# Optimization experiments

Measured on AMD Instinct MI355X. Metric: run time of the kernel, lower is better.

## Reference

```python
import jax, jax.numpy as jnp
import numpy as np
import math

B, T, IN_DIM = 4, 1024, 64
D, H, L, DFF = 1024, 16, 4, 4096
N_STEPS = 24
MAXLEN = 2048
DK = D // H


def _pos_encoding(max_len, d):
    pos = np.arange(max_len, dtype=np.float32)[:, None]
    div = np.exp(np.arange(0, d, 2, dtype=np.float32) * (-math.log(10000.0) / d))
    pe = np.zeros((max_len, d), dtype=np.float32)
    pe[:, 0::2] = np.sin(pos * div)
    pe[:, 1::2] = np.cos(pos * div)
    return jnp.asarray(pe)

_PE = _pos_encoding(MAXLEN, D)


def _lin(x, W, b):
    # torch Linear convention: W is (out, in)
    return x @ W.T + b


def _mha(q, kv, Wq, bq, Wk, bk, Wv, bv, Wo, bo):
    Bq, Tq, _ = q.shape
    Tk = kv.shape[1]
    Qh = _lin(q, Wq, bq).reshape(Bq, Tq, H, DK).transpose(0, 2, 1, 3)
    Kh = _lin(kv, Wk, bk).reshape(Bq, Tk, H, DK).transpose(0, 2, 1, 3)
    Vh = _lin(kv, Wv, bv).reshape(Bq, Tk, H, DK).transpose(0, 2, 1, 3)
    scores = jnp.einsum('bhqd,bhkd->bhqk', Qh, Kh) / math.sqrt(DK)
    probs = jax.nn.softmax(scores, axis=-1)
    out = jnp.einsum('bhqk,bhkd->bhqd', probs, Vh)
    out = out.transpose(0, 2, 1, 3).reshape(Bq, Tq, D)
    return _lin(out, Wo, bo)


def _ffn(x, W1, b1, W2, b2):
    return _lin(jax.nn.relu(_lin(x, W1, b1)), W2, b2)


def _ln(x, g, b, eps=1e-5):
    mu = jnp.mean(x, axis=-1, keepdims=True)
    var = jnp.var(x, axis=-1, keepdims=True)
    return (x - mu) / jnp.sqrt(var + eps) * g + b


def setup_inputs() -> dict:
    key = jax.random.key(0)
    ks = iter(jax.random.split(key, 64))
    def w(shape, s=0.02):
        return jax.random.normal(next(ks), shape, jnp.float32) * s
    inp = {'x': jax.random.normal(next(ks), (B, T, IN_DIM), jnp.float32)}
    inp['in_W'] = w((D, IN_DIM)); inp['in_b'] = jnp.zeros((D,), jnp.float32)
    for p in ['enc', 'dec']:
        for n in ['Wq', 'Wk', 'Wv', 'Wo']:
            inp[f'{p}_{n}'] = w((L, D, D))
            inp[f'{p}_b{n[1].lower()}'] = jnp.zeros((L, D), jnp.float32)
    for p in ['ffe', 'ffd']:
        inp[f'{p}_W1'] = w((DFF, D)); inp[f'{p}_b1'] = jnp.zeros((DFF,), jnp.float32)
        inp[f'{p}_W2'] = w((D, DFF)); inp[f'{p}_b2'] = jnp.zeros((D,), jnp.float32)
    for p in ['ne', 'nd']:
        inp[f'{p}_g'] = jnp.ones((D,), jnp.float32); inp[f'{p}_b'] = jnp.zeros((D,), jnp.float32)
    inp['out_W'] = w((1, D)); inp['out_b'] = jnp.zeros((1,), jnp.float32)
    inp['temb_W'] = w((D, 1)); inp['temb_b'] = jnp.zeros((D,), jnp.float32)
    return inp


def reference(x, in_W, in_b,
              enc_Wq, enc_bq, enc_Wk, enc_bk, enc_Wv, enc_bv, enc_Wo, enc_bo,
              ffe_W1, ffe_b1, ffe_W2, ffe_b2, ne_g, ne_b,
              dec_Wq, dec_bq, dec_Wk, dec_bk, dec_Wv, dec_bv, dec_Wo, dec_bo,
              ffd_W1, ffd_b1, ffd_W2, ffd_b2, nd_g, nd_b,
              out_W, out_b, temb_W, temb_b):
    batch, seq, _ = x.shape
    h = _lin(x, in_W, in_b) + _PE[:seq]
    for l in range(L):
        h = _mha(h, h, enc_Wq[l], enc_bq[l], enc_Wk[l], enc_bk[l],
                 enc_Wv[l], enc_bv[l], enc_Wo[l], enc_bo[l])
        h = _ln(h + _ffn(h, ffe_W1, ffe_b1, ffe_W2, ffe_b2), ne_g, ne_b)
    dec = jnp.zeros((batch, 1, D), x.dtype)
    preds = []
    for _ in range(N_STEPS):
        d = dec + _PE[:dec.shape[1]]
        for l in range(L):
            # same layer weights used for self- and cross-attention, as in source
            d = _mha(d, d, dec_Wq[l], dec_bq[l], dec_Wk[l], dec_bk[l],
                     dec_Wv[l], dec_bv[l], dec_Wo[l], dec_bo[l])
            d = _mha(d, h, dec_Wq[l], dec_bq[l], dec_Wk[l], dec_bk[l],
                     dec_Wv[l], dec_bv[l], dec_Wo[l], dec_bo[l])
            d = _ln(d + _ffn(d, ffd_W1, ffd_b1, ffd_W2, ffd_b2), nd_g, nd_b)
        step = _lin(d[:, -1, :], out_W, out_b)        # (B, 1)
        preds.append(step[:, None, :])                 # (B, 1, 1)
        emb = _lin(step, temb_W, temb_b)[:, None, :]   # (B, 1, D)
        dec = jnp.concatenate([dec, emb], axis=1)
    return jnp.concatenate(preds, axis=1)              # (B, n_steps, 1)
```

## Files before the change

### kernel.cpp

```cpp
#include <hip/hip_runtime.h>
#include <math.h>

#define DM    1024
#define NH    16
#define DKH   64
#define NL    4
#define DFFN  4096
#define BB    4
#define TT    1024
#define NSTEP 24
#define BT    (BB*TT)
#define MD    (BB*NSTEP)
#define CSPLIT 8
#define CKEYS  (TT/CSPLIT)

typedef __attribute__((ext_vector_type(8))) short s16x8;
typedef __attribute__((ext_vector_type(4))) short s16x4;
typedef __attribute__((ext_vector_type(4))) float f32x4;

__device__ inline short f2b(float f){
  unsigned u = __float_as_uint(f);
  u += 0x7fffu + ((u>>16)&1u);
  return (short)(u>>16);
}
__device__ inline float b2f(short h){
  return __uint_as_float(((unsigned)(unsigned short)h)<<16);
}

__global__ __launch_bounds__(256)
void split_kernel(const float* __restrict__ X, short* __restrict__ Hi,
                  short* __restrict__ Lo, int n8)
{
  const size_t i = (size_t)blockIdx.x*256 + threadIdx.x;
  if (i >= (size_t)n8) return;
  const float4 v0 = *(const float4*)(X + i*8);
  const float4 v1 = *(const float4*)(X + i*8 + 4);
  const float f[8] = {v0.x,v0.y,v0.z,v0.w,v1.x,v1.y,v1.z,v1.w};
  s16x8 hv, lv;
  #pragma unroll
  for (int e=0;e<8;e++){
    const short h = f2b(f[e]);
    hv[e] = h;
    lv[e] = f2b(f[e] - b2f(h));
  }
  *(s16x8*)(Hi + i*8) = hv;
  *(s16x8*)(Lo + i*8) = lv;
}

__global__ void zero_kernel(float* __restrict__ p, int n) {
  int i = blockIdx.x*256 + threadIdx.x;
  if (i < n) p[i] = 0.f;
}

__global__ __launch_bounds__(256)
void add_pe_split(const float* __restrict__ h, short* __restrict__ Hi,
                  short* __restrict__ Lo)
{
  const int row = blockIdx.x;
  const int pos = row & (TT-1);
  const int d = threadIdx.x*4;
  const float4 a = *(const float4*)(h + (size_t)row*DM + d);
  const float c1 = -9.210340371976184f / 1024.0f;
  const float e0 = expf((float)d * c1);
  const float e1 = expf((float)(d+2) * c1);
  const float a0 = (float)pos * e0, a1 = (float)pos * e1;
  const float v[4] = {a.x + sinf(a0), a.y + cosf(a0), a.z + sinf(a1), a.w + cosf(a1)};
  s16x4 hv, lv;
  #pragma unroll
  for (int e=0;e<4;e++){
    const short hb = f2b(v[e]);
    hv[e] = hb;
    lv[e] = f2b(v[e] - b2f(hb));
  }
  *(s16x4*)(Hi + (size_t)row*DM + d) = hv;
  *(s16x4*)(Lo + (size_t)row*DM + d) = lv;
}

__global__ __launch_bounds__(256)
void dec_prep_split(short* __restrict__ Dhi, short* __restrict__ Dlo,
                    const float* __restrict__ tok)
{
  const int r = blockIdx.x;
  const int i = r >> 2;
  const int d = threadIdx.x*4;
  const float4 a = *(const float4*)(tok + (size_t)r*DM + d);
  const float c1 = -9.210340371976184f / 1024.0f;
  const float e0 = expf((float)d * c1);
  const float e1 = expf((float)(d+2) * c1);
  const float a0 = (float)i * e0, a1 = (float)i * e1;
  const float v[4] = {a.x + sinf(a0), a.y + cosf(a0), a.z + sinf(a1), a.w + cosf(a1)};
  s16x4 hv, lv;
  #pragma unroll
  for (int e=0;e<4;e++){
    const short hb = f2b(v[e]);
    hv[e] = hb;
    lv[e] = f2b(v[e] - b2f(hb));
  }
  *(s16x4*)(Dhi + (size_t)r*DM + d) = hv;
  *(s16x4*)(Dlo + (size_t)r*DM + d) = lv;
}

template<int ACT, int OUT_MODE>
__global__ __launch_bounds__(256, 2)
void gemm_split(const short* __restrict__ Ahi, const short* __restrict__ Alo,
                const short* __restrict__ Bhi, const short* __restrict__ Blo,
                const float* __restrict__ bias,
                float* __restrict__ C, short* __restrict__ Chi, short* __restrict__ Clo,
                int M, int N, int K)
{
  __shared__ __align__(16) short lA[2][128][40];
  __shared__ __align__(16) short lB[2][128][40];
  const int tid = threadIdx.x;
  const int m0 = blockIdx.x*128, n0 = blockIdx.y*128;
  const int lane = tid & 63, w = tid >> 6;
  const int wr = w >> 1, wc = w & 1;
  const int fr = lane & 15, fq = lane >> 4;

  f32x4 acc[4][4];
  #pragma unroll
  for (int i=0;i<4;i++)
    #pragma unroll
    for (int j=0;j<4;j++) acc[i][j] = (f32x4){0.f,0.f,0.f,0.f};

  for (int k0 = 0; k0 < K; k0 += 32) {
    __syncthreads();
    #pragma unroll
    for (int j=0;j<2;j++){
      const int cc = tid + j*256;
      const int row = cc >> 2, kq = cc & 3;
      const size_t ga = (size_t)(m0+row)*K + k0 + kq*8;
      const size_t gb = (size_t)(n0+row)*K + k0 + kq*8;
      *(s16x8*)&lA[0][row][kq*8] = *(const s16x8*)(Ahi + ga);
      *(s16x8*)&lA[1][row][kq*8] = *(const s16x8*)(Alo + ga);
      *(s16x8*)&lB[0][row][kq*8] = *(const s16x8*)(Bhi + gb);
      *(s16x8*)&lB[1][row][kq*8] = *(const s16x8*)(Blo + gb);
    }
    __syncthreads();
    s16x8 ah[4], al[4], bh[4], bl[4];
    #pragma unroll
    for (int i=0;i<4;i++){
      ah[i] = *(const s16x8*)&lA[0][wr*64+i*16+fr][fq*8];
      al[i] = *(const s16x8*)&lA[1][wr*64+i*16+fr][fq*8];
    }
    #pragma unroll
    for (int j=0;j<4;j++){
      bh[j] = *(const s16x8*)&lB[0][wc*64+j*16+fr][fq*8];
      bl[j] = *(const s16x8*)&lB[1][wc*64+j*16+fr][fq*8];
    }
    #pragma unroll
    for (int i=0;i<4;i++)
      #pragma unroll
      for (int j=0;j<4;j++){
        acc[i][j] = __builtin_amdgcn_mfma_f32_16x16x32_bf16(ah[i], bh[j], acc[i][j], 0,0,0);
        acc[i][j] = __builtin_amdgcn_mfma_f32_16x16x32_bf16(ah[i], bl[j], acc[i][j], 0,0,0);
        acc[i][j] = __builtin_amdgcn_mfma_f32_16x16x32_bf16(al[i], bh[j], acc[i][j], 0,0,0);
      }
  }
  #pragma unroll
  for (int j=0;j<4;j++){
    const int col = n0 + wc*64 + j*16 + fr;
    const float bv = bias[col];
    #pragma unroll
    for (int i=0;i<4;i++){
      const int row0 = m0 + wr*64 + i*16 + fq*4;
      #pragma unroll
      for (int r=0;r<4;r++){
        float v = acc[i][j][r] + bv;
        if (ACT==1) v = fmaxf(v, 0.f);
        const size_t idx = (size_t)(row0+r)*N + col;
        if (OUT_MODE==0 || OUT_MODE==2) C[idx] = v;
        if (OUT_MODE==1 || OUT_MODE==2){
          const short hb = f2b(v);
          Chi[idx] = hb;
          Clo[idx] = f2b(v - b2f(hb));
        }
        if (OUT_MODE==3) Chi[idx] = f2b(v);
      }
    }
  }
}

template<int MR>
__global__ __launch_bounds__(256)
void gemm_dec(const short* __restrict__ Ahi, const short* __restrict__ Alo,
              const short* __restrict__ B0hi, const short* __restrict__ B0lo,
              const short* __restrict__ B1hi, const short* __restrict__ B1lo,
              const short* __restrict__ B2hi, const short* __restrict__ B2lo,
              float* __restrict__ part, int N, int K, int KS)
{
  const short* Bhi = (blockIdx.z==0) ? B0hi : (blockIdx.z==1 ? B1hi : B2hi);
  const short* Blo = (blockIdx.z==0) ? B0lo : (blockIdx.z==1 ? B1lo : B2lo);
  float* P = part + ((size_t)blockIdx.z*KS + blockIdx.y)*(size_t)MD*N;
  const int KK = K / KS;
  const int kbase = blockIdx.y * KK;
  const int n0 = blockIdx.x * 128;
  __shared__ __align__(16) short lA[2][96][40];
  __shared__ __align__(16) short lB[2][128][40];
  const int tid = threadIdx.x;
  const int lane = tid & 63, w = tid >> 6;
  const int fr = lane & 15, fq = lane >> 4;
  constexpr int CH = MR*128;

  f32x4 acc[MR][2];
  #pragma unroll
  for (int i=0;i<MR;i++){ acc[i][0]=(f32x4){0,0,0,0}; acc[i][1]=(f32x4){0,0,0,0}; }

  for (int k0 = kbase; k0 < kbase + KK; k0 += 32) {
    __syncthreads();
    #pragma unroll
    for (int t=0; t<(CH+255)/256; t++){
      const int cc = tid + t*256;
      if (cc < CH){
        const int row = cc>>3, hl = (cc>>2)&1, kq = cc&3;
        const short* src = hl ? Alo : Ahi;
        *(s16x8*)&lA[hl][row][kq*8] = *(const s16x8*)(src + (size_t)row*K + k0 + kq*8);
      }
    }
    #pragma unroll
    for (int t=0; t<4; t++){
      const int cc = tid + t*256;
      const int row = cc>>3, hl = (cc>>2)&1, kq = cc&3;
      const short* src = hl ? Blo : Bhi;
      *(s16x8*)&lB[hl][row][kq*8] = *(const s16x8*)(src + (size_t)(n0+row)*K + k0 + kq*8);
    }
    __syncthreads();
    s16x8 bh[2], bl[2];
    #pragma unroll
    for (int j=0;j<2;j++){
      bh[j] = *(const s16x8*)&lB[0][w*32+j*16+fr][fq*8];
      bl[j] = *(const s16x8*)&lB[1][w*32+j*16+fr][fq*8];
    }
    #pragma unroll
    for (int i=0;i<MR;i++){
      const s16x8 ah = *(const s16x8*)&lA[0][i*16+fr][fq*8];
      const s16x8 al = *(const s16x8*)&lA[1][i*16+fr][fq*8];
      #pragma unroll
      for (int j=0;j<2;j++){
        acc[i][j] = __builtin_amdgcn_mfma_f32_16x16x32_bf16(ah, bh[j], acc[i][j], 0,0,0);
        acc[i][j] = __builtin_amdgcn_mfma_f32_16x16x32_bf16(ah, bl[j], acc[i][j], 0,0,0);
        acc[i][j] = __builtin_amdgcn_mfma_f32_16x16x32_bf16(al, bh[j], acc[i][j], 0,0,0);
      }
    }
  }
  #pragma unroll
  for (int j=0;j<2;j++){
    const int col = n0 + w*32 + j*16 + fr;
    #pragma unroll
    for (int i=0;i<MR;i++){
      const int row0 = i*16 + fq*4;
      #pragma unroll
      for (int r=0;r<4;r++)
        P[(size_t)(row0+r)*N + col] = acc[i][j][r];
    }
  }
}

template<int ACT, int MODE>
__global__ __launch_bounds__(256)
void reduce_dec(const float* __restrict__ part,
                const float* __restrict__ b0, const float* __restrict__ b1,
                const float* __restrict__ b2,
                float* __restrict__ o0, float* __restrict__ o1, float* __restrict__ o2,
                short* __restrict__ ohi, short* __restrict__ olo,
                int N, int KS)
{
  const int idx = blockIdx.x*256 + threadIdx.x;
  const int z = blockIdx.y;
  const float* P = part + (size_t)z*KS*(size_t)MD*N;
  const float* bias = (z==0)?b0:(z==1?b1:b2);
  float* out = (z==0)?o0:(z==1?o1:o2);
  float s = 0.f;
  for (int ks=0; ks<KS; ks++) s += P[(size_t)ks*MD*N + idx];
  s += bias[idx & (N-1)];
  if (ACT==1) s = fmaxf(s, 0.f);
  if (MODE==0 || MODE==2) out[idx] = s;
  if (MODE==1 || MODE==2){
    if (z==0){
      const short hb = f2b(s);
      ohi[idx] = hb;
      olo[idx] = f2b(s - b2f(hb));
    }
  }
}

__global__ __launch_bounds__(256)
void attn_enc(const float* __restrict__ Qg, const float* __restrict__ Kg,
              const float* __restrict__ Vg, short* __restrict__ Ohi,
              short* __restrict__ Olo)
{
  const int bh = blockIdx.y;
  const int b = bh >> 4, hh = bh & 15;
  const int row = blockIdx.x*256 + threadIdx.x;
  const size_t base = ((size_t)b*TT)*DM + hh*DKH;
  float q[64];
  {
    const float* qp = Qg + base + (size_t)row*DM;
    #pragma unroll
    for (int d4=0; d4<16; d4++){
      const float4 v = *(const float4*)(qp + d4*4);
      q[d4*4+0]=v.x; q[d4*4+1]=v.y; q[d4*4+2]=v.z; q[d4*4+3]=v.w;
    }
  }
  float o[64];
  #pragma unroll
  for (int d=0;d<64;d++) o[d]=0.f;
  float m = -INFINITY, l = 0.f;
  __shared__ float Ks[64][68];
  __shared__ float Vs[64][68];
  for (int kt=0; kt<TT; kt+=64) {
    __syncthreads();
    #pragma unroll
    for (int t=0;t<4;t++){
      const int fi = threadIdx.x + t*256;
      const int j = fi>>4, dq = fi&15;
      *(float4*)&Ks[j][dq*4] = *(const float4*)(Kg + base + (size_t)(kt+j)*DM + dq*4);
      *(float4*)&Vs[j][dq*4] = *(const float4*)(Vg + base + (size_t)(kt+j)*DM + dq*4);
    }
    __syncthreads();
    for (int j=0;j<64;j++){
      float s0=0.f,s1=0.f,s2=0.f,s3=0.f;
      #pragma unroll
      for (int d=0; d<64; d+=4){
        s0 = fmaf(q[d+0], Ks[j][d+0], s0);
        s1 = fmaf(q[d+1], Ks[j][d+1], s1);
        s2 = fmaf(q[d+2], Ks[j][d+2], s2);
        s3 = fmaf(q[d+3], Ks[j][d+3], s3);
      }
      const float s = ((s0+s1)+(s2+s3)) * 0.125f;
      if (s > m) {
        const float f = __expf(m - s);
        l *= f;
        #pragma unroll
        for (int d=0;d<64;d++) o[d] *= f;
        m = s;
      }
      const float p = __expf(s - m);
      l += p;
      #pragma unroll
      for (int d=0;d<64;d++) o[d] = fmaf(p, Vs[j][d], o[d]);
    }
  }
  const float inv = 1.f / l;
  #pragma unroll
  for (int d8=0; d8<8; d8++){
    s16x8 hv, lv;
    #pragma unroll
    for (int e=0;e<8;e++){
      const float f = o[d8*8+e]*inv;
      const short hb = f2b(f);
      hv[e] = hb;
      lv[e] = f2b(f - b2f(hb));
    }
    *(s16x8*)(Ohi + base + (size_t)row*DM + d8*8) = hv;
    *(s16x8*)(Olo + base + (size_t)row*DM + d8*8) = lv;
  }
}

__global__ __launch_bounds__(256)
void attn_dec_selfp(const float* __restrict__ Qg, const float* __restrict__ Kg,
                    const float* __restrict__ Vg, short* __restrict__ Ohi,
                    short* __restrict__ Olo, int n)
{
  const int b = blockIdx.x >> 4, hh = blockIdx.x & 15;
  const size_t base = (size_t)b*DM + hh*DKH;
  __shared__ float Qs[NSTEP][68], Ks[NSTEP][68], Vs[NSTEP][68];
  __shared__ float P[NSTEP][28];
  const int tid = threadIdx.x;
  for (int t = tid; t < 3*n*16; t += 256) {
    const int tensor = t / (n*16);
    const int fi = t - tensor*(n*16);
    const int row = fi >> 4, dq = fi & 15;
    const float* src = (tensor==0?Qg:(tensor==1?Kg:Vg)) + base + (size_t)(row*4)*DM + dq*4;
    float (*dst)[68] = (tensor==0?Qs:(tensor==1?Ks:Vs));
    *(float4*)&dst[row][dq*4] = *(const float4*)src;
  }
  __syncthreads();
  for (int idx = tid; idx < n*n; idx += 256) {
    const int i = idx / n, j = idx - i*n;
    float s0=0.f,s1=0.f,s2=0.f,s3=0.f;
    #pragma unroll
    for (int d=0; d<64; d+=4){
      s0 = fmaf(Qs[i][d+0], Ks[j][d+0], s0);
      s1 = fmaf(Qs[i][d+1], Ks[j][d+1], s1);
      s2 = fmaf(Qs[i][d+2], Ks[j][d+2], s2);
      s3 = fmaf(Qs[i][d+3], Ks[j][d+3], s3);
    }
    P[i][j] = ((s0+s1)+(s2+s3))*0.125f;
  }
  __syncthreads();
  if (tid < n) {
    float mm = -INFINITY;
    for (int j=0;j<n;j++) mm = fmaxf(mm, P[tid][j]);
    float l = 0.f;
    for (int j=0;j<n;j++){ const float p = __expf(P[tid][j]-mm); P[tid][j]=p; l+=p; }
    const float inv = 1.f/l;
    for (int j=0;j<n;j++) P[tid][j] *= inv;
  }
  __syncthreads();
  for (int idx = tid; idx < n*64; idx += 256){
    const int i = idx >> 6, d = idx & 63;
    float s = 0.f;
    for (int j=0;j<n;j++) s = fmaf(P[i][j], Vs[j][d], s);
    const short hb = f2b(s);
    const size_t o = base + (size_t)(i*4)*DM + d;
    Ohi[o] = hb;
    Olo[o] = f2b(s - b2f(hb));
  }
}

__global__ __launch_bounds__(256)
void attn_cross_part(const float* __restrict__ Qg, const short* __restrict__ Kc,
                     const short* __restrict__ Vc, float* __restrict__ opart,
                     float* __restrict__ mlpart, int n)
{
  const int ks = blockIdx.x;
  const int bh = blockIdx.y;
  const int b = bh >> 4, hh = bh & 15;
  __shared__ float Qs[NSTEP][68];
  __shared__ float KVs[CKEYS][68];
  __shared__ float S[NSTEP][CKEYS+4];
  const int tid = threadIdx.x;
  const size_t qbase = (size_t)b*DM + hh*DKH;
  for (int t=tid; t<n*16; t+=256){
    const int row = t>>4, dq = t&15;
    *(float4*)&Qs[row][dq*4] = *(const float4*)(Qg + qbase + (size_t)(row*4)*DM + dq*4);
  }
  const size_t kbase = ((size_t)b*TT + (size_t)ks*CKEYS)*DM + hh*DKH;
  for (int t=tid; t<CKEYS*8; t+=256){
    const int row = t>>3, d8 = t&7;
    const s16x8 v = *(const s16x8*)(Kc + kbase + (size_t)row*DM + d8*8);
    #pragma unroll
    for (int e=0;e<8;e++) KVs[row][d8*8+e] = b2f(v[e]);
  }
  __syncthreads();
  for (int idx=tid; idx<n*128; idx+=256){
    const int i = idx >> 7, j = idx & 127;
    float s0=0.f,s1=0.f,s2=0.f,s3=0.f;
    #pragma unroll
    for (int d=0; d<64; d+=4){
      s0 = fmaf(Qs[i][d+0], KVs[j][d+0], s0);
      s1 = fmaf(Qs[i][d+1], KVs[j][d+1], s1);
      s2 = fmaf(Qs[i][d+2], KVs[j][d+2], s2);
      s3 = fmaf(Qs[i][d+3], KVs[j][d+3], s3);
    }
    S[i][j] = ((s0+s1)+(s2+s3))*0.125f;
  }
  __syncthreads();
  for (int t=tid; t<CKEYS*8; t+=256){
    const int row = t>>3, d8 = t&7;
    const s16x8 v = *(const s16x8*)(Vc + kbase + (size_t)row*DM + d8*8);
    #pragma unroll
    for (int e=0;e<8;e++) KVs[row][d8*8+e] = b2f(v[e]);
  }
  if (tid < n){
    float mm=-INFINITY;
    for (int j=0;j<CKEYS;j++) mm = fmaxf(mm, S[tid][j]);
    float l=0.f;
    for (int j=0;j<CKEYS;j++){ const float p=__expf(S[tid][j]-mm); S[tid][j]=p; l+=p; }
    mlpart[((size_t)bh*CSPLIT+ks)*(2*NSTEP) + tid*2+0] = mm;
    mlpart[((size_t)bh*CSPLIT+ks)*(2*NSTEP) + tid*2+1] = l;
  }
  __syncthreads();
  for (int idx=tid; idx<n*64; idx+=256){
    const int i = idx >> 6, d = idx & 63;
    float s=0.f;
    for (int j=0;j<CKEYS;j++) s = fmaf(S[i][j], KVs[j][d], s);
    opart[(((size_t)bh*CSPLIT+ks)*NSTEP + i)*DKH + d] = s;
  }
}

__global__ __launch_bounds__(256)
void attn_cross_comb(const float* __restrict__ opart, const float* __restrict__ mlpart,
                     short* __restrict__ Ohi, short* __restrict__ Olo, int n)
{
  const int bh = blockIdx.x;
  const int idx = blockIdx.y*256 + threadIdx.x;
  const int i = idx >> 6, d = idx & 63;
  if (i >= n) return;
  float M = -INFINITY;
  #pragma unroll
  for (int s=0;s<CSPLIT;s++)
    M = fmaxf(M, mlpart[((size_t)bh*CSPLIT+s)*(2*NSTEP) + i*2]);
  float acc = 0.f, L = 0.f;
  #pragma unroll
  for (int s=0;s<CSPLIT;s++){
    const float mm = mlpart[((size_t)bh*CSPLIT+s)*(2*NSTEP) + i*2+0];
    const float ll = mlpart[((size_t)bh*CSPLIT+s)*(2*NSTEP) + i*2+1];
    const float f = __expf(mm - M);
    acc = fmaf(f, opart[(((size_t)bh*CSPLIT+s)*NSTEP + i)*DKH + d], acc);
    L   = fmaf(f, ll, L);
  }
  const int b = bh >> 4, hh = bh & 15;
  const float v = acc / L;
  const short hb = f2b(v);
  const size_t o = ((size_t)(i*4+b))*DM + hh*DKH + d;
  Ohi[o] = hb;
  Olo[o] = f2b(v - b2f(hb));
}

__device__ inline float wave_sum(float v){
  #pragma unroll
  for (int off=1; off<64; off<<=1) v += __shfl_xor(v, off, 64);
  return v;
}

__global__ __launch_bounds__(256)
void ln_add_split(const float* __restrict__ X, const float* __restrict__ Y,
                  const float* __restrict__ g, const float* __restrict__ be,
                  short* __restrict__ Ohi, short* __restrict__ Olo)
{
  const size_t row = blockIdx.x;
  const int tid = threadIdx.x;
  const float4 a = *(const float4*)(X + row*DM + tid*4);
  const float4 b = *(const float4*)(Y + row*DM + tid*4);
  const float v0=a.x+b.x, v1=a.y+b.y, v2=a.z+b.z, v3=a.w+b.w;
  float s = v0+v1+v2+v3;
  float q = v0*v0+v1*v1+v2*v2+v3*v3;
  s = wave_sum(s); q = wave_sum(q);
  __shared__ float rs[4], rq[4];
  if ((tid&63)==0){ rs[tid>>6]=s; rq[tid>>6]=q; }
  __syncthreads();
  const float S = rs[0]+rs[1]+rs[2]+rs[3];
  const float Q = rq[0]+rq[1]+rq[2]+rq[3];
  const float mean = S * (1.f/DM);
  const float var  = Q * (1.f/DM) - mean*mean;
  const float rstd = rsqrtf(var + 1e-5f);
  const float4 gv = *(const float4*)(g  + tid*4);
  const float4 bv = *(const float4*)(be + tid*4);
  const float v[4] = {(v0-mean)*rstd*gv.x + bv.x, (v1-mean)*rstd*gv.y + bv.y,
                      (v2-mean)*rstd*gv.z + bv.z, (v3-mean)*rstd*gv.w + bv.w};
  s16x4 hv, lv;
  #pragma unroll
  for (int e=0;e<4;e++){
    const short hb = f2b(v[e]);
    hv[e] = hb;
    lv[e] = f2b(v[e] - b2f(hb));
  }
  *(s16x4*)(Ohi + row*DM + tid*4) = hv;
  *(s16x4*)(Olo + row*DM + tid*4) = lv;
}

__global__ __launch_bounds__(256)
void ln_add_dec(const float* __restrict__ X, const float* __restrict__ Y,
                const float* __restrict__ g, const float* __restrict__ be,
                float* __restrict__ Outf, short* __restrict__ Ohi,
                short* __restrict__ Olo)
{
  const size_t row = blockIdx.x;
  const int tid = threadIdx.x;
  const float4 a = *(const float4*)(X + row*DM + tid*4);
  const float4 b = *(const float4*)(Y + row*DM + tid*4);
  const float v0=a.x+b.x, v1=a.y+b.y, v2=a.z+b.z, v3=a.w+b.w;
  float s = v0+v1+v2+v3;
  float q = v0*v0+v1*v1+v2*v2+v3*v3;
  s = wave_sum(s); q = wave_sum(q);
  __shared__ float rs[4], rq[4];
  if ((tid&63)==0){ rs[tid>>6]=s; rq[tid>>6]=q; }
  __syncthreads();
  const float S = rs[0]+rs[1]+rs[2]+rs[3];
  const float Q = rq[0]+rq[1]+rq[2]+rq[3];
  const float mean = S * (1.f/DM);
  const float var  = Q * (1.f/DM) - mean*mean;
  const float rstd = rsqrtf(var + 1e-5f);
  const float4 gv = *(const float4*)(g  + tid*4);
  const float4 bv = *(const float4*)(be + tid*4);
  const float v[4] = {(v0-mean)*rstd*gv.x + bv.x, (v1-mean)*rstd*gv.y + bv.y,
                      (v2-mean)*rstd*gv.z + bv.z, (v3-mean)*rstd*gv.w + bv.w};
  float4 of; of.x=v[0]; of.y=v[1]; of.z=v[2]; of.w=v[3];
  *(float4*)(Outf + row*DM + tid*4) = of;
  s16x4 hv, lv;
  #pragma unroll
  for (int e=0;e<4;e++){
    const short hb = f2b(v[e]);
    hv[e] = hb;
    lv[e] = f2b(v[e] - b2f(hb));
  }
  *(s16x4*)(Ohi + row*DM + tid*4) = hv;
  *(s16x4*)(Olo + row*DM + tid*4) = lv;
}

__global__ __launch_bounds__(256)
void out_step(const float* __restrict__ Dv, const float* __restrict__ outW,
              const float* __restrict__ outB, const float* __restrict__ tembW,
              const float* __restrict__ tembB, float* __restrict__ dout,
              float* __restrict__ tok, int s)
{
  const int b = blockIdx.x;
  const int tid = threadIdx.x;
  const float* drow = Dv + ((size_t)(s*4 + b))*DM;
  const float4 dv = *(const float4*)(drow + tid*4);
  const float4 wv = *(const float4*)(outW + tid*4);
  float part = dv.x*wv.x + dv.y*wv.y + dv.z*wv.z + dv.w*wv.w;
  part = wave_sum(part);
  __shared__ float red[4];
  __shared__ float stepv;
  if ((tid&63)==0) red[tid>>6] = part;
  __syncthreads();
  if (tid==0) stepv = red[0]+red[1]+red[2]+red[3] + outB[0];
  __syncthreads();
  const float sv = stepv;
  if (tid==0) dout[b*NSTEP + s] = sv;
  if (s+1 < NSTEP) {
    const int d = tid*4;
    const float4 tw = *(const float4*)(tembW + d);
    const float4 tb = *(const float4*)(tembB + d);
    float4 e;
    e.x = fmaf(sv, tw.x, tb.x); e.y = fmaf(sv, tw.y, tb.y);
    e.z = fmaf(sv, tw.z, tb.z); e.w = fmaf(sv, tw.w, tb.w);
    *(float4*)(tok + ((size_t)((s+1)*4 + b))*DM + d) = e;
  }
}

extern "C" void kernel_launch(void* const* d_in, const int* in_sizes, int n_in,
                              void* d_out, int out_size, void* d_ws, size_t ws_size,
                              hipStream_t stream)
{
  (void)in_sizes; (void)n_in; (void)out_size; (void)ws_size;
  const float* x      = (const float*)d_in[0];
  const float* in_W   = (const float*)d_in[1];
  const float* in_b   = (const float*)d_in[2];
  const float* enc_Wq = (const float*)d_in[3];
  const float* enc_bq = (const float*)d_in[4];
  const float* enc_Wk = (const float*)d_in[5];
  const float* enc_bk = (const float*)d_in[6];
  const float* enc_Wv = (const float*)d_in[7];
  const float* enc_bv = (const float*)d_in[8];
  const float* enc_Wo = (const float*)d_in[9];
  const float* enc_bo = (const float*)d_in[10];
  const float* dec_Wq = (const float*)d_in[11];
  const float* dec_bq = (const float*)d_in[12];
  const float* dec_Wk = (const float*)d_in[13];
  const float* dec_bk = (const float*)d_in[14];
  const float* dec_Wv = (const float*)d_in[15];
  const float* dec_bv = (const float*)d_in[16];
  const float* dec_Wo = (const float*)d_in[17];
  const float* dec_bo = (const float*)d_in[18];
  const float* ffe_W1 = (const float*)d_in[19];
  const float* ffe_b1 = (const float*)d_in[20];
  const float* ffe_W2 = (const float*)d_in[21];
  const float* ffe_b2 = (const float*)d_in[22];
  const float* ffd_W1 = (const float*)d_in[23];
  const float* ffd_b1 = (const float*)d_in[24];
  const float* ffd_W2 = (const float*)d_in[25];
  const float* ffd_b2 = (const float*)d_in[26];
  const float* ne_g   = (const float*)d_in[27];
  const float* ne_b   = (const float*)d_in[28];
  const float* nd_g   = (const float*)d_in[29];
  const float* nd_b   = (const float*)d_in[30];
  const float* out_W  = (const float*)d_in[31];
  const float* out_b  = (const float*)d_in[32];
  const float* temb_W = (const float*)d_in[33];
  const float* temb_b = (const float*)d_in[34];
  float* dout = (float*)d_out;

  float* ws = (float*)d_ws;
  size_t off = 0;
  auto alloc  = [&](size_t n){ n = (n+3)&~(size_t)3; float* p = ws + off; off += n; return p; };
  auto allocS = [&](size_t n){ size_t nf = ((n+1)/2 + 3)&~(size_t)3; short* p = (short*)(ws + off); off += nf; return p; };

  short* hshi = allocS((size_t)BT*DM);
  short* hslo = allocS((size_t)BT*DM);
  float* h    = alloc((size_t)BT*DM);
  float* hn   = h;
  float* t0   = alloc((size_t)BT*DM);
  float* t1   = alloc((size_t)BT*DM);
  float* t2   = alloc((size_t)BT*DM);
  short* t3hi = allocS((size_t)BT*DM);
  short* t3lo = allocS((size_t)BT*DM);
  short* hnhi = allocS((size_t)BT*DM);
  short* hnlo = allocS((size_t)BT*DM);
  float* t4   = alloc((size_t)BT*DM);
  float* part = t4;
  short* fmhi = (short*)t0;
  short* fmlo = fmhi + (size_t)BT*DFFN;
  short* kcb  = allocS((size_t)NL*BT*DM);
  short* vcb  = allocS((size_t)NL*BT*DM);
  short* xshi = allocS((size_t)BT*64);
  short* xslo = allocS((size_t)BT*64);
  short* iwhi = allocS((size_t)DM*64);
  short* iwlo = allocS((size_t)DM*64);
  short* w0hi = allocS((size_t)DM*DM); short* w0lo = allocS((size_t)DM*DM);
  short* w1hi = allocS((size_t)DM*DM); short* w1lo = allocS((size_t)DM*DM);
  short* w2hi = allocS((size_t)DM*DM); short* w2lo = allocS((size_t)DM*DM);
  short* w3hi = allocS((size_t)DM*DM); short* w3lo = allocS((size_t)DM*DM);
  short* wfhi = allocS((size_t)DFFN*DM); short* wflo = allocS((size_t)DFFN*DM);
  float* tok  = alloc((size_t)MD*DM);
  float* dbuf = alloc((size_t)MD*DM);
  float* dq   = alloc((size_t)MD*DM);
  float* dk   = alloc((size_t)MD*DM);
  float* dv_  = alloc((size_t)MD*DM);
  float* dffo = alloc((size_t)MD*DM);
  short* dbhi = allocS((size_t)MD*DM);  short* dblo = allocS((size_t)MD*DM);
  short* dahi = allocS((size_t)MD*DM);  short* dalo = allocS((size_t)MD*DM);
  short* dmhi = allocS((size_t)MD*DFFN);short* dmlo = allocS((size_t)MD*DFFN);
  float* opart= alloc((size_t)BB*NH*CSPLIT*NSTEP*DKH);
  float* mlp  = alloc((size_t)BB*NH*CSPLIT*2*NSTEP);

  const size_t MM = (size_t)DM*DM;
  short* dwq = (short*)t0;
  short* dwk = (short*)t1;
  short* dwv = (short*)t2;
  short* dwo = (short*)h;
  short* fw1h = t3hi; short* fw1l = t3lo;
  short* fw2h = hnhi; short* fw2l = hnlo;

  auto cvt = [&](const float* src, short* hi, short* lo, size_t n){
    split_kernel<<<(int)((n/8 + 255)/256), 256, 0, stream>>>(src, hi, lo, (int)(n/8));
  };

  cvt(x,    xshi, xslo, (size_t)BT*64);
  cvt(in_W, iwhi, iwlo, (size_t)DM*64);
  zero_kernel<<<(MD*DM+255)/256, 256, 0, stream>>>(tok, MD*DM);

  gemm_split<0,0><<<dim3(BT/128, DM/128), 256, 0, stream>>>(
      xshi, xslo, iwhi, iwlo, in_b, h, (short*)nullptr, (short*)nullptr, BT, DM, 64);
  add_pe_split<<<BT, 256, 0, stream>>>(h, hshi, hslo);

  for (int l=0; l<NL; ++l) {
    const size_t wo = (size_t)l*DM*DM, bo_ = (size_t)l*DM;
    cvt(enc_Wq+wo, w0hi, w0lo, MM);
    cvt(enc_Wk+wo, w1hi, w1lo, MM);
    cvt(enc_Wv+wo, w2hi, w2lo, MM);
    cvt(enc_Wo+wo, w3hi, w3lo, MM);
    gemm_split<0,0><<<dim3(32,8),256,0,stream>>>(hshi, hslo, w0hi, w0lo, enc_bq+bo_,
        t0, (short*)nullptr, (short*)nullptr, BT, DM, DM);
    gemm_split<0,0><<<dim3(32,8),256,0,stream>>>(hshi, hslo, w1hi, w1lo, enc_bk+bo_,
        t1, (short*)nullptr, (short*)nullptr, BT, DM, DM);
    gemm_split<0,0><<<dim3(32,8),256,0,stream>>>(hshi, hslo, w2hi, w2lo, enc_bv+bo_,
        t2, (short*)nullptr, (short*)nullptr, BT, DM, DM);
    attn_enc<<<dim3(TT/256, BB*NH),256,0,stream>>>(t0, t1, t2, t3hi, t3lo);
    gemm_split<0,2><<<dim3(32,8),256,0,stream>>>(t3hi, t3lo, w3hi, w3lo, enc_bo+bo_,
        hn, hnhi, hnlo, BT, DM, DM);
    cvt(ffe_W1, wfhi, wflo, (size_t)DFFN*DM);
    gemm_split<1,1><<<dim3(32,32),256,0,stream>>>(hnhi, hnlo, wfhi, wflo, ffe_b1,
        (float*)nullptr, fmhi, fmlo, BT, DFFN, DM);
    cvt(ffe_W2, wfhi, wflo, (size_t)DM*DFFN);
    gemm_split<0,0><<<dim3(32,8),256,0,stream>>>(fmhi, fmlo, wfhi, wflo, ffe_b2,
        t4, (short*)nullptr, (short*)nullptr, BT, DM, DFFN);
    ln_add_split<<<BT,256,0,stream>>>(hn, t4, ne_g, ne_b, hshi, hslo);
  }

  for (int l=0; l<NL; ++l) {
    const size_t wo = (size_t)l*DM*DM, bo_ = (size_t)l*DM;
    cvt(dec_Wk+wo, w0hi, w0lo, MM);
    cvt(dec_Wv+wo, w1hi, w1lo, MM);
    gemm_split<0,3><<<dim3(32,8),256,0,stream>>>(hshi, hslo, w0hi, w0lo, dec_bk+bo_,
        (float*)nullptr, kcb+(size_t)l*BT*DM, (short*)nullptr, BT, DM, DM);
    gemm_split<0,3><<<dim3(32,8),256,0,stream>>>(hshi, hslo, w1hi, w1lo, dec_bv+bo_,
        (float*)nullptr, vcb+(size_t)l*BT*DM, (short*)nullptr, BT, DM, DM);
  }

  for (int l=0; l<NL; ++l) {
    const size_t wo = (size_t)l*DM*DM;
    cvt(dec_Wq+wo, dwq + (size_t)l*2*MM, dwq + (size_t)l*2*MM + MM, MM);
    cvt(dec_Wk+wo, dwk + (size_t)l*2*MM, dwk + (size_t)l*2*MM + MM, MM);
    cvt(dec_Wv+wo, dwv + (size_t)l*2*MM, dwv + (size_t)l*2*MM + MM, MM);
    cvt(dec_Wo+wo, dwo + (size_t)l*2*MM, dwo + (size_t)l*2*MM + MM, MM);
  }
  cvt(ffd_W1, fw1h, fw1l, (size_t)DFFN*DM);
  cvt(ffd_W2, fw2h, fw2l, (size_t)DM*DFFN);

  #define GD(MRv, grid, ...) do { switch(MRv){ \
    case 1: gemm_dec<1><<<grid,256,0,stream>>>(__VA_ARGS__); break; \
    case 2: gemm_dec<2><<<grid,256,0,stream>>>(__VA_ARGS__); break; \
    case 3: gemm_dec<3><<<grid,256,0,stream>>>(__VA_ARGS__); break; \
    case 4: gemm_dec<4><<<grid,256,0,stream>>>(__VA_ARGS__); break; \
    case 5: gemm_dec<5><<<grid,256,0,stream>>>(__VA_ARGS__); break; \
    default: gemm_dec<6><<<grid,256,0,stream>>>(__VA_ARGS__); break; } } while(0)

  for (int s=0; s<NSTEP; ++s) {
    const int n = s+1;
    const int rows = 4*n;
    const int Mt = (rows + 15) & ~15;
    const int MR = Mt >> 4;
    dec_prep_split<<<rows,256,0,stream>>>(dbhi, dblo, tok);
    for (int l=0; l<NL; ++l) {
      const size_t bo_ = (size_t)l*DM;
      short* qh = dwq + (size_t)l*2*MM; short* ql = qh + MM;
      short* kh = dwk + (size_t)l*2*MM; short* kl = kh + MM;
      short* vh = dwv + (size_t)l*2*MM; short* vl = vh + MM;
      short* oh = dwo + (size_t)l*2*MM; short* ol = oh + MM;
      GD(MR, dim3(8,8,3), dbhi,dblo, qh,ql, kh,kl, vh,vl, part, DM, DM, 8);
      reduce_dec<0,0><<<dim3(Mt*4,3),256,0,stream>>>(part, dec_bq+bo_, dec_bk+bo_, dec_bv+bo_,
          dq, dk, dv_, (short*)nullptr, (short*)nullptr, DM, 8);
      attn_dec_selfp<<<BB*NH,256,0,stream>>>(dq, dk, dv_, dahi, dalo, n);
      GD(MR, dim3(8,8,1), dahi,dalo, oh,ol, oh,ol, oh,ol, part, DM, DM, 8);
      reduce_dec<0,1><<<dim3(Mt*4,1),256,0,stream>>>(part, dec_bo+bo_, dec_bo+bo_, dec_bo+bo_,
          (float*)nullptr,(float*)nullptr,(float*)nullptr, dbhi, dblo, DM, 8);
      GD(MR, dim3(8,8,1), dbhi,dblo, qh,ql, qh,ql, qh,ql, part, DM, DM, 8);
      reduce_dec<0,0><<<dim3(Mt*4,1),256,0,stream>>>(part, dec_bq+bo_, dec_bq+bo_, dec_bq+bo_,
          dq, dq, dq, (short*)nullptr, (short*)nullptr, DM, 8);
      attn_cross_part<<<dim3(CSPLIT, BB*NH),256,0,stream>>>(dq, kcb+(size_t)l*BT*DM,
          vcb+(size_t)l*BT*DM, opart, mlp, n);
      attn_cross_comb<<<dim3(BB*NH, 6),256,0,stream>>>(opart, mlp, dahi, dalo, n);
      GD(MR, dim3(8,8,1), dahi,dalo, oh,ol, oh,ol, oh,ol, part, DM, DM, 8);
      reduce_dec<0,2><<<dim3(Mt*4,1),256,0,stream>>>(part, dec_bo+bo_, dec_bo+bo_, dec_bo+bo_,
          dbuf, dbuf, dbuf, dbhi, dblo, DM, 8);
      GD(MR, dim3(32,8,1), dbhi,dblo, fw1h,fw1l, fw1h,fw1l, fw1h,fw1l, part, DFFN, DM, 8);
      reduce_dec<1,1><<<dim3(Mt*16,1),256,0,stream>>>(part, ffd_b1, ffd_b1, ffd_b1,
          (float*)nullptr,(float*)nullptr,(float*)nullptr, dmhi, dmlo, DFFN, 8);
      GD(MR, dim3(8,16,1), dmhi,dmlo, fw2h,fw2l, fw2h,fw2l, fw2h,fw2l, part, DM, DFFN, 16);
      reduce_dec<0,0><<<dim3(Mt*4,1),256,0,stream>>>(part, ffd_b2, ffd_b2, ffd_b2,
          dffo, dffo, dffo, (short*)nullptr, (short*)nullptr, DM, 16);
      ln_add_dec<<<rows,256,0,stream>>>(dbuf, dffo, nd_g, nd_b, dbuf, dbhi, dblo);
    }
    out_step<<<BB,256,0,stream>>>(dbuf, out_W, out_b, temb_W, temb_b, dout, tok, s);
  }
  #undef GD
}
```

Before: 16.50 ms.

## Fuse decoder loop into one persistent kernel with grid-wide barriers

Replaces the per-step, per-layer chain of small decoder kernels (split-K GEMMs, reductions, attention, layernorm, output step) with a single persistent kernel of 96 blocks. Stages are separated by software grid barriers built on an atomic counter. The aim is to remove the cost of well over a thousand kernel launches and the split-K partial-sum round trips. In exchange, the GEMMs run on only 16–64 blocks with the full K per block and always cover 96 rows regardless of step, which cuts parallelism and adds barrier spin overhead.

```diff
diff --git a/kernel.cpp b/kernel.cpp
--- a/kernel.cpp
+++ b/kernel.cpp
@@ -13,6 +13,7 @@
 #define MD    (BB*NSTEP)
 #define CSPLIT 8
 #define CKEYS  (TT/CSPLIT)
+#define NB    96
 
 typedef __attribute__((ext_vector_type(8))) short s16x8;
 typedef __attribute__((ext_vector_type(4))) short s16x4;
@@ -25,6 +26,12 @@
 }
 __device__ inline float b2f(short h){
   return __uint_as_float(((unsigned)(unsigned short)h)<<16);
+}
+
+__device__ inline float wave_sum(float v){
+  #pragma unroll
+  for (int off=1; off<64; off<<=1) v += __shfl_xor(v, off, 64);
+  return v;
 }
 
 __global__ __launch_bounds__(256)
@@ -50,6 +57,10 @@
 __global__ void zero_kernel(float* __restrict__ p, int n) {
   int i = blockIdx.x*256 + threadIdx.x;
   if (i < n) p[i] = 0.f;
+}
+
+__global__ void zero_u32(unsigned* __restrict__ p) {
+  if (threadIdx.x==0 && blockIdx.x==0) *p = 0u;
 }
 
 __global__ __launch_bounds__(256)
@@ -74,30 +85,6 @@
   }
   *(s16x4*)(Hi + (size_t)row*DM + d) = hv;
   *(s16x4*)(Lo + (size_t)row*DM + d) = lv;
-}
-
-__global__ __launch_bounds__(256)
-void dec_prep_split(short* __restrict__ Dhi, short* __restrict__ Dlo,
-                    const float* __restrict__ tok)
-{
-  const int r = blockIdx.x;
-  const int i = r >> 2;
-  const int d = threadIdx.x*4;
-  const float4 a = *(const float4*)(tok + (size_t)r*DM + d);
-  const float c1 = -9.210340371976184f / 1024.0f;
-  const float e0 = expf((float)d * c1);
-  const float e1 = expf((float)(d+2) * c1);
-  const float a0 = (float)i * e0, a1 = (float)i * e1;
-  const float v[4] = {a.x + sinf(a0), a.y + cosf(a0), a.z + sinf(a1), a.w + cosf(a1)};
-  s16x4 hv, lv;
-  #pragma unroll
-  for (int e=0;e<4;e++){
-    const short hb = f2b(v[e]);
-    hv[e] = hb;
-    lv[e] = f2b(v[e] - b2f(hb));
-  }
-  *(s16x4*)(Dhi + (size_t)r*DM + d) = hv;
-  *(s16x4*)(Dlo + (size_t)r*DM + d) = lv;
 }
 
 template<int ACT, int OUT_MODE>
@@ -176,109 +163,6 @@
         }
         if (OUT_MODE==3) Chi[idx] = f2b(v);
       }
-    }
-  }
-}
-
-template<int MR>
-__global__ __launch_bounds__(256)
-void gemm_dec(const short* __restrict__ Ahi, const short* __restrict__ Alo,
-              const short* __restrict__ B0hi, const short* __restrict__ B0lo,
-              const short* __restrict__ B1hi, const short* __restrict__ B1lo,
-              const short* __restrict__ B2hi, const short* __restrict__ B2lo,
-              float* __restrict__ part, int N, int K, int KS)
-{
-  const short* Bhi = (blockIdx.z==0) ? B0hi : (blockIdx.z==1 ? B1hi : B2hi);
-  const short* Blo = (blockIdx.z==0) ? B0lo : (blockIdx.z==1 ? B1lo : B2lo);
-  float* P = part + ((size_t)blockIdx.z*KS + blockIdx.y)*(size_t)MD*N;
-  const int KK = K / KS;
-  const int kbase = blockIdx.y * KK;
-  const int n0 = blockIdx.x * 128;
-  __shared__ __align__(16) short lA[2][96][40];
-  __shared__ __align__(16) short lB[2][128][40];
-  const int tid = threadIdx.x;
-  const int lane = tid & 63, w = tid >> 6;
-  const int fr = lane & 15, fq = lane >> 4;
-  constexpr int CH = MR*128;
-
-  f32x4 acc[MR][2];
-  #pragma unroll
-  for (int i=0;i<MR;i++){ acc[i][0]=(f32x4){0,0,0,0}; acc[i][1]=(f32x4){0,0,0,0}; }
-
-  for (int k0 = kbase; k0 < kbase + KK; k0 += 32) {
-    __syncthreads();
-    #pragma unroll
-    for (int t=0; t<(CH+255)/256; t++){
-      const int cc = tid + t*256;
-      if (cc < CH){
-        const int row = cc>>3, hl = (cc>>2)&1, kq = cc&3;
-        const short* src = hl ? Alo : Ahi;
-        *(s16x8*)&lA[hl][row][kq*8] = *(const s16x8*)(src + (size_t)row*K + k0 + kq*8);
-      }
-    }
-    #pragma unroll
-    for (int t=0; t<4; t++){
-      const int cc = tid + t*256;
-      const int row = cc>>3, hl = (cc>>2)&1, kq = cc&3;
-      const short* src = hl ? Blo : Bhi;
-      *(s16x8*)&lB[hl][row][kq*8] = *(const s16x8*)(src + (size_t)(n0+row)*K + k0 + kq*8);
-    }
-    __syncthreads();
-    s16x8 bh[2], bl[2];
-    #pragma unroll
-    for (int j=0;j<2;j++){
-      bh[j] = *(const s16x8*)&lB[0][w*32+j*16+fr][fq*8];
-      bl[j] = *(const s16x8*)&lB[1][w*32+j*16+fr][fq*8];
-    }
-    #pragma unroll
-    for (int i=0;i<MR;i++){
-      const s16x8 ah = *(const s16x8*)&lA[0][i*16+fr][fq*8];
-      const s16x8 al = *(const s16x8*)&lA[1][i*16+fr][fq*8];
-      #pragma unroll
-      for (int j=0;j<2;j++){
-        acc[i][j] = __builtin_amdgcn_mfma_f32_16x16x32_bf16(ah, bh[j], acc[i][j], 0,0,0);
-        acc[i][j] = __builtin_amdgcn_mfma_f32_16x16x32_bf16(ah, bl[j], acc[i][j], 0,0,0);
-        acc[i][j] = __builtin_amdgcn_mfma_f32_16x16x32_bf16(al, bh[j], acc[i][j], 0,0,0);
-      }
-    }
-  }
-  #pragma unroll
-  for (int j=0;j<2;j++){
-    const int col = n0 + w*32 + j*16 + fr;
-    #pragma unroll
-    for (int i=0;i<MR;i++){
-      const int row0 = i*16 + fq*4;
-      #pragma unroll
-      for (int r=0;r<4;r++)
-        P[(size_t)(row0+r)*N + col] = acc[i][j][r];
-    }
-  }
-}
-
-template<int ACT, int MODE>
-__global__ __launch_bounds__(256)
-void reduce_dec(const float* __restrict__ part,
-                const float* __restrict__ b0, const float* __restrict__ b1,
-                const float* __restrict__ b2,
-                float* __restrict__ o0, float* __restrict__ o1, float* __restrict__ o2,
-                short* __restrict__ ohi, short* __restrict__ olo,
-                int N, int KS)
-{
-  const int idx = blockIdx.x*256 + threadIdx.x;
-  const int z = blockIdx.y;
-  const float* P = part + (size_t)z*KS*(size_t)MD*N;
-  const float* bias = (z==0)?b0:(z==1?b1:b2);
-  float* out = (z==0)?o0:(z==1?o1:o2);
-  float s = 0.f;
-  for (int ks=0; ks<KS; ks++) s += P[(size_t)ks*MD*N + idx];
-  s += bias[idx & (N-1)];
-  if (ACT==1) s = fmaxf(s, 0.f);
-  if (MODE==0 || MODE==2) out[idx] = s;
-  if (MODE==1 || MODE==2){
-    if (z==0){
-      const short hb = f2b(s);
-      ohi[idx] = hb;
-      olo[idx] = f2b(s - b2f(hb));
     }
   }
 }
@@ -357,154 +241,6 @@
 }
 
 __global__ __launch_bounds__(256)
-void attn_dec_selfp(const float* __restrict__ Qg, const float* __restrict__ Kg,
-                    const float* __restrict__ Vg, short* __restrict__ Ohi,
-                    short* __restrict__ Olo, int n)
-{
-  const int b = blockIdx.x >> 4, hh = blockIdx.x & 15;
-  const size_t base = (size_t)b*DM + hh*DKH;
-  __shared__ float Qs[NSTEP][68], Ks[NSTEP][68], Vs[NSTEP][68];
-  __shared__ float P[NSTEP][28];
-  const int tid = threadIdx.x;
-  for (int t = tid; t < 3*n*16; t += 256) {
-    const int tensor = t / (n*16);
-    const int fi = t - tensor*(n*16);
-    const int row = fi >> 4, dq = fi & 15;
-    const float* src = (tensor==0?Qg:(tensor==1?Kg:Vg)) + base + (size_t)(row*4)*DM + dq*4;
-    float (*dst)[68] = (tensor==0?Qs:(tensor==1?Ks:Vs));
-    *(float4*)&dst[row][dq*4] = *(const float4*)src;
-  }
-  __syncthreads();
-  for (int idx = tid; idx < n*n; idx += 256) {
-    const int i = idx / n, j = idx - i*n;
-    float s0=0.f,s1=0.f,s2=0.f,s3=0.f;
-    #pragma unroll
-    for (int d=0; d<64; d+=4){
-      s0 = fmaf(Qs[i][d+0], Ks[j][d+0], s0);
-      s1 = fmaf(Qs[i][d+1], Ks[j][d+1], s1);
-      s2 = fmaf(Qs[i][d+2], Ks[j][d+2], s2);
-      s3 = fmaf(Qs[i][d+3], Ks[j][d+3], s3);
-    }
-    P[i][j] = ((s0+s1)+(s2+s3))*0.125f;
-  }
-  __syncthreads();
-  if (tid < n) {
-    float mm = -INFINITY;
-    for (int j=0;j<n;j++) mm = fmaxf(mm, P[tid][j]);
-    float l = 0.f;
-    for (int j=0;j<n;j++){ const float p = __expf(P[tid][j]-mm); P[tid][j]=p; l+=p; }
-    const float inv = 1.f/l;
-    for (int j=0;j<n;j++) P[tid][j] *= inv;
-  }
-  __syncthreads();
-  for (int idx = tid; idx < n*64; idx += 256){
-    const int i = idx >> 6, d = idx & 63;
-    float s = 0.f;
-    for (int j=0;j<n;j++) s = fmaf(P[i][j], Vs[j][d], s);
-    const short hb = f2b(s);
-    const size_t o = base + (size_t)(i*4)*DM + d;
-    Ohi[o] = hb;
-    Olo[o] = f2b(s - b2f(hb));
-  }
-}
-
-__global__ __launch_bounds__(256)
-void attn_cross_part(const float* __restrict__ Qg, const short* __restrict__ Kc,
-                     const short* __restrict__ Vc, float* __restrict__ opart,
-                     float* __restrict__ mlpart, int n)
-{
-  const int ks = blockIdx.x;
-  const int bh = blockIdx.y;
-  const int b = bh >> 4, hh = bh & 15;
-  __shared__ float Qs[NSTEP][68];
-  __shared__ float KVs[CKEYS][68];
-  __shared__ float S[NSTEP][CKEYS+4];
-  const int tid = threadIdx.x;
-  const size_t qbase = (size_t)b*DM + hh*DKH;
-  for (int t=tid; t<n*16; t+=256){
-    const int row = t>>4, dq = t&15;
-    *(float4*)&Qs[row][dq*4] = *(const float4*)(Qg + qbase + (size_t)(row*4)*DM + dq*4);
-  }
-  const size_t kbase = ((size_t)b*TT + (size_t)ks*CKEYS)*DM + hh*DKH;
-  for (int t=tid; t<CKEYS*8; t+=256){
-    const int row = t>>3, d8 = t&7;
-    const s16x8 v = *(const s16x8*)(Kc + kbase + (size_t)row*DM + d8*8);
-    #pragma unroll
-    for (int e=0;e<8;e++) KVs[row][d8*8+e] = b2f(v[e]);
-  }
-  __syncthreads();
-  for (int idx=tid; idx<n*128; idx+=256){
-    const int i = idx >> 7, j = idx & 127;
-    float s0=0.f,s1=0.f,s2=0.f,s3=0.f;
-    #pragma unroll
-    for (int d=0; d<64; d+=4){
-      s0 = fmaf(Qs[i][d+0], KVs[j][d+0], s0);
-      s1 = fmaf(Qs[i][d+1], KVs[j][d+1], s1);
-      s2 = fmaf(Qs[i][d+2], KVs[j][d+2], s2);
-      s3 = fmaf(Qs[i][d+3], KVs[j][d+3], s3);
-    }
-    S[i][j] = ((s0+s1)+(s2+s3))*0.125f;
-  }
-  __syncthreads();
-  for (int t=tid; t<CKEYS*8; t+=256){
-    const int row = t>>3, d8 = t&7;
-    const s16x8 v = *(const s16x8*)(Vc + kbase + (size_t)row*DM + d8*8);
-    #pragma unroll
-    for (int e=0;e<8;e++) KVs[row][d8*8+e] = b2f(v[e]);
-  }
-  if (tid < n){
-    float mm=-INFINITY;
-    for (int j=0;j<CKEYS;j++) mm = fmaxf(mm, S[tid][j]);
-    float l=0.f;
-    for (int j=0;j<CKEYS;j++){ const float p=__expf(S[tid][j]-mm); S[tid][j]=p; l+=p; }
-    mlpart[((size_t)bh*CSPLIT+ks)*(2*NSTEP) + tid*2+0] = mm;
-    mlpart[((size_t)bh*CSPLIT+ks)*(2*NSTEP) + tid*2+1] = l;
-  }
-  __syncthreads();
-  for (int idx=tid; idx<n*64; idx+=256){
-    const int i = idx >> 6, d = idx & 63;
-    float s=0.f;
-    for (int j=0;j<CKEYS;j++) s = fmaf(S[i][j], KVs[j][d], s);
-    opart[(((size_t)bh*CSPLIT+ks)*NSTEP + i)*DKH + d] = s;
-  }
-}
-
-__global__ __launch_bounds__(256)
-void attn_cross_comb(const float* __restrict__ opart, const float* __restrict__ mlpart,
-                     short* __restrict__ Ohi, short* __restrict__ Olo, int n)
-{
-  const int bh = blockIdx.x;
-  const int idx = blockIdx.y*256 + threadIdx.x;
-  const int i = idx >> 6, d = idx & 63;
-  if (i >= n) return;
-  float M = -INFINITY;
-  #pragma unroll
-  for (int s=0;s<CSPLIT;s++)
-    M = fmaxf(M, mlpart[((size_t)bh*CSPLIT+s)*(2*NSTEP) + i*2]);
-  float acc = 0.f, L = 0.f;
-  #pragma unroll
-  for (int s=0;s<CSPLIT;s++){
-    const float mm = mlpart[((size_t)bh*CSPLIT+s)*(2*NSTEP) + i*2+0];
-    const float ll = mlpart[((size_t)bh*CSPLIT+s)*(2*NSTEP) + i*2+1];
-    const float f = __expf(mm - M);
-    acc = fmaf(f, opart[(((size_t)bh*CSPLIT+s)*NSTEP + i)*DKH + d], acc);
-    L   = fmaf(f, ll, L);
-  }
-  const int b = bh >> 4, hh = bh & 15;
-  const float v = acc / L;
-  const short hb = f2b(v);
-  const size_t o = ((size_t)(i*4+b))*DM + hh*DKH + d;
-  Ohi[o] = hb;
-  Olo[o] = f2b(v - b2f(hb));
-}
-
-__device__ inline float wave_sum(float v){
-  #pragma unroll
-  for (int off=1; off<64; off<<=1) v += __shfl_xor(v, off, 64);
-  return v;
-}
-
-__global__ __launch_bounds__(256)
 void ln_add_split(const float* __restrict__ X, const float* __restrict__ Y,
                   const float* __restrict__ g, const float* __restrict__ be,
                   short* __restrict__ Ohi, short* __restrict__ Olo)
@@ -540,21 +276,259 @@
   *(s16x4*)(Olo + row*DM + tid*4) = lv;
 }
 
-__global__ __launch_bounds__(256)
-void ln_add_dec(const float* __restrict__ X, const float* __restrict__ Y,
-                const float* __restrict__ g, const float* __restrict__ be,
-                float* __restrict__ Outf, short* __restrict__ Ohi,
-                short* __restrict__ Olo)
-{
-  const size_t row = blockIdx.x;
+
+__device__ inline void gsync(unsigned* bar, unsigned target){
+  __syncthreads();
+  if (threadIdx.x == 0){
+    __threadfence();
+    __hip_atomic_fetch_add(bar, 1u, __ATOMIC_RELAXED, __HIP_MEMORY_SCOPE_AGENT);
+    while (__hip_atomic_load(bar, __ATOMIC_RELAXED, __HIP_MEMORY_SCOPE_AGENT) < target)
+      __builtin_amdgcn_s_sleep(2);
+    __threadfence();
+  }
+  __syncthreads();
+}
+
+__device__ inline void gemm_unit(
+    const short* __restrict__ Ahi, const short* __restrict__ Alo,
+    const short* __restrict__ Bhi, const short* __restrict__ Blo,
+    const float* __restrict__ bias, int n0, int N, int K, int kbase, int KK,
+    int mode, int act,
+    float* __restrict__ Cf, short* __restrict__ Chi, short* __restrict__ Clo,
+    char* smem)
+{
+  short (*lA)[96][40] = (short(*)[96][40])smem;
+  short (*lB)[64][40] = (short(*)[64][40])(smem + 15360);
+  const int tid = threadIdx.x, lane = tid & 63, w = tid >> 6;
+  const int fr = lane & 15, fq = lane >> 4;
+  f32x4 a0={0.f,0.f,0.f,0.f}, a1=a0, a2=a0, a3=a0, a4=a0, a5=a0;
+  for (int k0 = kbase; k0 < kbase + KK; k0 += 32){
+    __syncthreads();
+    #pragma unroll
+    for (int t=0;t<3;t++){
+      const int cc = tid + t*256;
+      const int row = cc>>3, hl=(cc>>2)&1, kq=cc&3;
+      const short* src = hl ? Alo : Ahi;
+      *(s16x8*)&lA[hl][row][kq*8] = *(const s16x8*)(src + (size_t)row*K + k0 + kq*8);
+    }
+    #pragma unroll
+    for (int t=0;t<2;t++){
+      const int cc = tid + t*256;
+      const int row = cc>>3, hl=(cc>>2)&1, kq=cc&3;
+      const short* src = hl ? Blo : Bhi;
+      *(s16x8*)&lB[hl][row][kq*8] = *(const s16x8*)(src + (size_t)(n0+row)*K + k0 + kq*8);
+    }
+    __syncthreads();
+    const s16x8 bh = *(const s16x8*)&lB[0][w*16+fr][fq*8];
+    const s16x8 bl = *(const s16x8*)&lB[1][w*16+fr][fq*8];
+    #define MSTEP(i, A) { const s16x8 ah=*(const s16x8*)&lA[0][(i)*16+fr][fq*8]; \
+                          const s16x8 al=*(const s16x8*)&lA[1][(i)*16+fr][fq*8]; \
+                          A=__builtin_amdgcn_mfma_f32_16x16x32_bf16(ah,bh,A,0,0,0); \
+                          A=__builtin_amdgcn_mfma_f32_16x16x32_bf16(ah,bl,A,0,0,0); \
+                          A=__builtin_amdgcn_mfma_f32_16x16x32_bf16(al,bh,A,0,0,0); }
+    MSTEP(0,a0) MSTEP(1,a1) MSTEP(2,a2) MSTEP(3,a3) MSTEP(4,a4) MSTEP(5,a5)
+    #undef MSTEP
+  }
+  const int col = n0 + w*16 + fr;
+  const float bv = bias ? bias[col] : 0.f;
+  const f32x4 accs[6] = {a0,a1,a2,a3,a4,a5};
+  #pragma unroll
+  for (int i=0;i<6;i++){
+    const int row0 = i*16 + fq*4;
+    #pragma unroll
+    for (int r=0;r<4;r++){
+      float v = accs[i][r] + bv;
+      if (act) v = fmaxf(v, 0.f);
+      const size_t idx = (size_t)(row0+r)*N + col;
+      if (mode==0 || mode==2) Cf[idx] = v;
+      if (mode==1 || mode==2){
+        const short hb = f2b(v);
+        Chi[idx] = hb;
+        Clo[idx] = f2b(v - b2f(hb));
+      }
+    }
+  }
+}
+
+__device__ inline void prep_unit(short* __restrict__ Dhi, short* __restrict__ Dlo,
+                                 const float* __restrict__ tok, int r)
+{
+  const int i = r >> 2;
+  const int d = threadIdx.x*4;
+  const float4 a = *(const float4*)(tok + (size_t)r*DM + d);
+  const float c1 = -9.210340371976184f / 1024.0f;
+  const float e0 = expf((float)d * c1);
+  const float e1 = expf((float)(d+2) * c1);
+  const float a0 = (float)i * e0, a1 = (float)i * e1;
+  const float v[4] = {a.x + sinf(a0), a.y + cosf(a0), a.z + sinf(a1), a.w + cosf(a1)};
+  s16x4 hv, lv;
+  #pragma unroll
+  for (int e=0;e<4;e++){
+    const short hb = f2b(v[e]);
+    hv[e] = hb;
+    lv[e] = f2b(v[e] - b2f(hb));
+  }
+  *(s16x4*)(Dhi + (size_t)r*DM + d) = hv;
+  *(s16x4*)(Dlo + (size_t)r*DM + d) = lv;
+}
+
+__device__ inline void attn_self_unit(const float* __restrict__ Qg,
+    const float* __restrict__ Kg, const float* __restrict__ Vg,
+    short* __restrict__ Ohi, short* __restrict__ Olo, int n, int bh, char* smem)
+{
+  const int b = bh >> 4, hh = bh & 15;
+  const size_t base = (size_t)b*DM + hh*DKH;
+  float (*Qs)[68] = (float(*)[68])smem;
+  float (*Ks)[68] = (float(*)[68])(smem + 6528);
+  float (*Vs)[68] = (float(*)[68])(smem + 13056);
+  float (*P)[28]  = (float(*)[28])(smem + 19584);
   const int tid = threadIdx.x;
-  const float4 a = *(const float4*)(X + row*DM + tid*4);
-  const float4 b = *(const float4*)(Y + row*DM + tid*4);
-  const float v0=a.x+b.x, v1=a.y+b.y, v2=a.z+b.z, v3=a.w+b.w;
+  for (int t = tid; t < 3*n*16; t += 256){
+    const int tensor = t / (n*16);
+    const int fi = t - tensor*(n*16);
+    const int row = fi >> 4, dq4 = fi & 15;
+    const float* src = (tensor==0?Qg:(tensor==1?Kg:Vg)) + base + (size_t)(row*4)*DM + dq4*4;
+    float (*dst)[68] = (tensor==0?Qs:(tensor==1?Ks:Vs));
+    *(float4*)&dst[row][dq4*4] = *(const float4*)src;
+  }
+  __syncthreads();
+  for (int idx = tid; idx < n*n; idx += 256){
+    const int i = idx / n, j = idx - i*n;
+    float s0=0.f,s1=0.f,s2=0.f,s3=0.f;
+    #pragma unroll
+    for (int d=0; d<64; d+=4){
+      s0 = fmaf(Qs[i][d+0], Ks[j][d+0], s0);
+      s1 = fmaf(Qs[i][d+1], Ks[j][d+1], s1);
+      s2 = fmaf(Qs[i][d+2], Ks[j][d+2], s2);
+      s3 = fmaf(Qs[i][d+3], Ks[j][d+3], s3);
+    }
+    P[i][j] = ((s0+s1)+(s2+s3))*0.125f;
+  }
+  __syncthreads();
+  if (tid < n){
+    float mm = -INFINITY;
+    for (int j=0;j<n;j++) mm = fmaxf(mm, P[tid][j]);
+    float l = 0.f;
+    for (int j=0;j<n;j++){ const float p = __expf(P[tid][j]-mm); P[tid][j]=p; l+=p; }
+    const float inv = 1.f/l;
+    for (int j=0;j<n;j++) P[tid][j] *= inv;
+  }
+  __syncthreads();
+  for (int idx = tid; idx < n*64; idx += 256){
+    const int i = idx >> 6, d = idx & 63;
+    float s = 0.f;
+    for (int j=0;j<n;j++) s = fmaf(P[i][j], Vs[j][d], s);
+    const short hb = f2b(s);
+    const size_t o = base + (size_t)(i*4)*DM + d;
+    Ohi[o] = hb;
+    Olo[o] = f2b(s - b2f(hb));
+  }
+}
+
+__device__ inline void cross_part_unit(const float* __restrict__ Qg,
+    const short* __restrict__ Kc, const short* __restrict__ Vc,
+    float* __restrict__ opart, float* __restrict__ mlpart, int n, int unit, char* smem)
+{
+  const int ks = unit & (CSPLIT-1), bh = unit >> 3;
+  const int b = bh >> 4, hh = bh & 15;
+  float (*Qs)[68]  = (float(*)[68])smem;
+  short (*KVs)[72] = (short(*)[72])(smem + 6528);
+  float (*S)[132]  = (float(*)[132])(smem + 24960);
+  const int tid = threadIdx.x;
+  __syncthreads();
+  const size_t qbase = (size_t)b*DM + hh*DKH;
+  for (int t=tid; t<n*16; t+=256){
+    const int row = t>>4, dq4 = t&15;
+    *(float4*)&Qs[row][dq4*4] = *(const float4*)(Qg + qbase + (size_t)(row*4)*DM + dq4*4);
+  }
+  const size_t kbase = ((size_t)b*TT + (size_t)ks*CKEYS)*DM + hh*DKH;
+  for (int t=tid; t<CKEYS*8; t+=256){
+    const int row = t>>3, d8 = t&7;
+    *(s16x8*)&KVs[row][d8*8] = *(const s16x8*)(Kc + kbase + (size_t)row*DM + d8*8);
+  }
+  __syncthreads();
+  for (int idx=tid; idx<n*128; idx+=256){
+    const int i = idx >> 7, j = idx & 127;
+    float s0=0.f,s1=0.f,s2=0.f,s3=0.f;
+    #pragma unroll
+    for (int d=0; d<64; d+=4){
+      s0 = fmaf(Qs[i][d+0], b2f(KVs[j][d+0]), s0);
+      s1 = fmaf(Qs[i][d+1], b2f(KVs[j][d+1]), s1);
+      s2 = fmaf(Qs[i][d+2], b2f(KVs[j][d+2]), s2);
+      s3 = fmaf(Qs[i][d+3], b2f(KVs[j][d+3]), s3);
+    }
+    S[i][j] = ((s0+s1)+(s2+s3))*0.125f;
+  }
+  __syncthreads();
+  for (int t=tid; t<CKEYS*8; t+=256){
+    const int row = t>>3, d8 = t&7;
+    *(s16x8*)&KVs[row][d8*8] = *(const s16x8*)(Vc + kbase + (size_t)row*DM + d8*8);
+  }
+  if (tid < n){
+    float mm=-INFINITY;
+    for (int j=0;j<CKEYS;j++) mm = fmaxf(mm, S[tid][j]);
+    float l=0.f;
+    for (int j=0;j<CKEYS;j++){ const float p=__expf(S[tid][j]-mm); S[tid][j]=p; l+=p; }
+    mlpart[((size_t)bh*CSPLIT+ks)*(2*NSTEP) + tid*2+0] = mm;
+    mlpart[((size_t)bh*CSPLIT+ks)*(2*NSTEP) + tid*2+1] = l;
+  }
+  __syncthreads();
+  for (int idx=tid; idx<n*64; idx+=256){
+    const int i = idx >> 6, d = idx & 63;
+    float s=0.f;
+    for (int j=0;j<CKEYS;j++) s = fmaf(S[i][j], b2f(KVs[j][d]), s);
+    opart[(((size_t)bh*CSPLIT+ks)*NSTEP + i)*DKH + d] = s;
+  }
+}
+
+__device__ inline void comb_unit(const float* __restrict__ opart,
+    const float* __restrict__ mlp, short* __restrict__ Ohi, short* __restrict__ Olo,
+    int n, int bh)
+{
+  const int b = bh >> 4, hh = bh & 15;
+  for (int idx=threadIdx.x; idx<n*64; idx+=256){
+    const int i = idx >> 6, d = idx & 63;
+    float M = -INFINITY;
+    #pragma unroll
+    for (int s=0;s<CSPLIT;s++)
+      M = fmaxf(M, mlp[((size_t)bh*CSPLIT+s)*(2*NSTEP) + i*2]);
+    float acc = 0.f, L = 0.f;
+    #pragma unroll
+    for (int s=0;s<CSPLIT;s++){
+      const float mm = mlp[((size_t)bh*CSPLIT+s)*(2*NSTEP) + i*2+0];
+      const float ll = mlp[((size_t)bh*CSPLIT+s)*(2*NSTEP) + i*2+1];
+      const float f = __expf(mm - M);
+      acc = fmaf(f, opart[(((size_t)bh*CSPLIT+s)*NSTEP + i)*DKH + d], acc);
+      L   = fmaf(f, ll, L);
+    }
+    const float v = acc / L;
+    const short hb = f2b(v);
+    const size_t o = ((size_t)(i*4+b))*DM + hh*DKH + d;
+    Ohi[o] = hb;
+    Olo[o] = f2b(v - b2f(hb));
+  }
+}
+
+__device__ inline void ln_unit(const float* __restrict__ part, const float* __restrict__ bias,
+    const float* __restrict__ X, const float* __restrict__ g, const float* __restrict__ be,
+    float* __restrict__ Outf, short* __restrict__ Ohi, short* __restrict__ Olo,
+    int row, char* smem)
+{
+  float* rs = (float*)smem;
+  float* rq = rs + 4;
+  const int tid = threadIdx.x;
+  float a0=0.f,a1=0.f,a2=0.f,a3=0.f;
+  #pragma unroll
+  for (int ks=0; ks<4; ks++){
+    const float4 p = *(const float4*)(part + ((size_t)ks*MD + row)*DM + tid*4);
+    a0+=p.x; a1+=p.y; a2+=p.z; a3+=p.w;
+  }
+  const float4 bvv = *(const float4*)(bias + tid*4);
+  const float4 xv  = *(const float4*)(X + (size_t)row*DM + tid*4);
+  const float v0=a0+bvv.x+xv.x, v1=a1+bvv.y+xv.y, v2=a2+bvv.z+xv.z, v3=a3+bvv.w+xv.w;
   float s = v0+v1+v2+v3;
   float q = v0*v0+v1*v1+v2*v2+v3*v3;
   s = wave_sum(s); q = wave_sum(q);
-  __shared__ float rs[4], rq[4];
   if ((tid&63)==0){ rs[tid>>6]=s; rq[tid>>6]=q; }
   __syncthreads();
   const float S = rs[0]+rs[1]+rs[2]+rs[3];
@@ -563,11 +537,11 @@
   const float var  = Q * (1.f/DM) - mean*mean;
   const float rstd = rsqrtf(var + 1e-5f);
   const float4 gv = *(const float4*)(g  + tid*4);
-  const float4 bv = *(const float4*)(be + tid*4);
-  const float v[4] = {(v0-mean)*rstd*gv.x + bv.x, (v1-mean)*rstd*gv.y + bv.y,
-                      (v2-mean)*rstd*gv.z + bv.z, (v3-mean)*rstd*gv.w + bv.w};
+  const float4 bv2 = *(const float4*)(be + tid*4);
+  const float v[4] = {(v0-mean)*rstd*gv.x + bv2.x, (v1-mean)*rstd*gv.y + bv2.y,
+                      (v2-mean)*rstd*gv.z + bv2.z, (v3-mean)*rstd*gv.w + bv2.w};
   float4 of; of.x=v[0]; of.y=v[1]; of.z=v[2]; of.w=v[3];
-  *(float4*)(Outf + row*DM + tid*4) = of;
+  *(float4*)(Outf + (size_t)row*DM + tid*4) = of;
   s16x4 hv, lv;
   #pragma unroll
   for (int e=0;e<4;e++){
@@ -575,32 +549,33 @@
     hv[e] = hb;
     lv[e] = f2b(v[e] - b2f(hb));
   }
-  *(s16x4*)(Ohi + row*DM + tid*4) = hv;
-  *(s16x4*)(Olo + row*DM + tid*4) = lv;
-}
-
-__global__ __launch_bounds__(256)
-void out_step(const float* __restrict__ Dv, const float* __restrict__ outW,
-              const float* __restrict__ outB, const float* __restrict__ tembW,
-              const float* __restrict__ tembB, float* __restrict__ dout,
-              float* __restrict__ tok, int s)
-{
-  const int b = blockIdx.x;
+  *(s16x4*)(Ohi + (size_t)row*DM + tid*4) = hv;
+  *(s16x4*)(Olo + (size_t)row*DM + tid*4) = lv;
+}
+
+__device__ inline void out_unit(const float* __restrict__ Dv, const float* __restrict__ outW,
+    const float* __restrict__ outB, const float* __restrict__ tembW,
+    const float* __restrict__ tembB, float* __restrict__ dout, float* __restrict__ tok,
+    int s, int b, char* smem)
+{
+  float* red = (float*)smem;
+  float* stepv = red + 4;
   const int tid = threadIdx.x;
   const float* drow = Dv + ((size_t)(s*4 + b))*DM;
-  const float4 dv = *(const float4*)(drow + tid*4);
+  const float4 dv4 = *(const float4*)(drow + tid*4);
   const float4 wv = *(const float4*)(outW + tid*4);
-  float part = dv.x*wv.x + dv.y*wv.y + dv.z*wv.z + dv.w*wv.w;
-  part = wave_sum(part);
-  __shared__ float red[4];
-  __shared__ float stepv;
-  if ((tid&63)==0) red[tid>>6] = part;
-  __syncthreads();
-  if (tid==0) stepv = red[0]+red[1]+red[2]+red[3] + outB[0];
-  __syncthreads();
-  const float sv = stepv;
-  if (tid==0) dout[b*NSTEP + s] = sv;
-  if (s+1 < NSTEP) {
+  float p = dv4.x*wv.x + dv4.y*wv.y + dv4.z*wv.z + dv4.w*wv.w;
+  p = wave_sum(p);
+  if ((tid&63)==0) red[tid>>6] = p;
+  __syncthreads();
+  if (tid==0){
+    const float sv = red[0]+red[1]+red[2]+red[3] + outB[0];
+    stepv[0] = sv;
+    dout[b*NSTEP + s] = sv;
+  }
+  __syncthreads();
+  const float sv = stepv[0];
+  if (s+1 < NSTEP){
     const int d = tid*4;
     const float4 tw = *(const float4*)(tembW + d);
     const float4 tb = *(const float4*)(tembB + d);
@@ -608,6 +583,91 @@
     e.x = fmaf(sv, tw.x, tb.x); e.y = fmaf(sv, tw.y, tb.y);
     e.z = fmaf(sv, tw.z, tb.z); e.w = fmaf(sv, tw.w, tb.w);
     *(float4*)(tok + ((size_t)((s+1)*4 + b))*DM + d) = e;
+  }
+}
+
+__global__ __launch_bounds__(256, 1)
+void dec_persist(const short* __restrict__ dwq, const short* __restrict__ dwk,
+                 const short* __restrict__ dwv, const short* __restrict__ dwo,
+                 const short* __restrict__ fw1h, const short* __restrict__ fw1l,
+                 const short* __restrict__ fw2h, const short* __restrict__ fw2l,
+                 const float* __restrict__ bq, const float* __restrict__ bk,
+                 const float* __restrict__ bv, const float* __restrict__ bo,
+                 const float* __restrict__ fb1, const float* __restrict__ fb2,
+                 const short* __restrict__ kcb, const short* __restrict__ vcb,
+                 const float* __restrict__ nd_g, const float* __restrict__ nd_b,
+                 const float* __restrict__ outW, const float* __restrict__ outB,
+                 const float* __restrict__ tembW, const float* __restrict__ tembB,
+                 float* __restrict__ dout, float* __restrict__ tok,
+                 float* __restrict__ dbuf, float* __restrict__ dq,
+                 float* __restrict__ dk, float* __restrict__ dv,
+                 short* __restrict__ dbhi, short* __restrict__ dblo,
+                 short* __restrict__ dahi, short* __restrict__ dalo,
+                 short* __restrict__ dmhi, short* __restrict__ dmlo,
+                 float* __restrict__ part, float* __restrict__ opart,
+                 float* __restrict__ mlp, unsigned* __restrict__ bar)
+{
+  __shared__ __align__(16) char smem[38912];
+  const int bid = blockIdx.x;
+  unsigned gen = 0;
+  const size_t MM = (size_t)DM*DM;
+  for (int s=0; s<NSTEP; ++s){
+    const int n = s+1, rows = 4*n;
+    prep_unit(dbhi, dblo, tok, bid);
+    gsync(bar, (++gen)*NB);
+    for (int l=0; l<NL; ++l){
+      const short* qh = dwq + (size_t)l*2*MM; const short* ql = qh + MM;
+      const short* kh = dwk + (size_t)l*2*MM; const short* kl = kh + MM;
+      const short* vh = dwv + (size_t)l*2*MM; const short* vl = vh + MM;
+      const short* oh = dwo + (size_t)l*2*MM; const short* ol = oh + MM;
+      const float* lbq = bq + (size_t)l*DM;
+      const float* lbk = bk + (size_t)l*DM;
+      const float* lbv = bv + (size_t)l*DM;
+      const float* lbo = bo + (size_t)l*DM;
+      if (bid < 48){
+        const int wsel = bid >> 4, t = bid & 15;
+        gemm_unit(dbhi, dblo,
+                  wsel==0?qh:(wsel==1?kh:vh), wsel==0?ql:(wsel==1?kl:vl),
+                  wsel==0?lbq:(wsel==1?lbk:lbv), t*64, DM, DM, 0, DM, 0, 0,
+                  wsel==0?dq:(wsel==1?dk:dv), nullptr, nullptr, smem);
+      }
+      gsync(bar, (++gen)*NB);
+      if (bid < 64) attn_self_unit(dq, dk, dv, dahi, dalo, n, bid, smem);
+      gsync(bar, (++gen)*NB);
+      if (bid < 16)
+        gemm_unit(dahi, dalo, oh, ol, lbo, bid*64, DM, DM, 0, DM, 1, 0,
+                  nullptr, dbhi, dblo, smem);
+      gsync(bar, (++gen)*NB);
+      if (bid < 16)
+        gemm_unit(dbhi, dblo, qh, ql, lbq, bid*64, DM, DM, 0, DM, 0, 0,
+                  dq, nullptr, nullptr, smem);
+      gsync(bar, (++gen)*NB);
+      for (int u=bid; u<64*CSPLIT; u+=NB)
+        cross_part_unit(dq, kcb + (size_t)l*BT*DM, vcb + (size_t)l*BT*DM,
+                        opart, mlp, n, u, smem);
+      gsync(bar, (++gen)*NB);
+      if (bid < 64) comb_unit(opart, mlp, dahi, dalo, n, bid);
+      gsync(bar, (++gen)*NB);
+      if (bid < 16)
+        gemm_unit(dahi, dalo, oh, ol, lbo, bid*64, DM, DM, 0, DM, 2, 0,
+                  dbuf, dbhi, dblo, smem);
+      gsync(bar, (++gen)*NB);
+      if (bid < 64)
+        gemm_unit(dbhi, dblo, fw1h, fw1l, fb1, bid*64, DFFN, DM, 0, DM, 1, 1,
+                  nullptr, dmhi, dmlo, smem);
+      gsync(bar, (++gen)*NB);
+      if (bid < 64){
+        const int ks = bid & 3, t = bid >> 2;
+        gemm_unit(dmhi, dmlo, fw2h, fw2l, nullptr, t*64, DM, DFFN, ks*1024, 1024, 0, 0,
+                  part + (size_t)ks*MD*DM, nullptr, nullptr, smem);
+      }
+      gsync(bar, (++gen)*NB);
+      if (bid < rows)
+        ln_unit(part, fb2, dbuf, nd_g, nd_b, dbuf, dbhi, dblo, bid, smem);
+      gsync(bar, (++gen)*NB);
+    }
+    if (bid < BB) out_unit(dbuf, outW, outB, tembW, tembB, dout, tok, s, bid, smem);
+    gsync(bar, (++gen)*NB);
   }
 }
 
@@ -689,12 +749,12 @@
   float* dq   = alloc((size_t)MD*DM);
   float* dk   = alloc((size_t)MD*DM);
   float* dv_  = alloc((size_t)MD*DM);
-  float* dffo = alloc((size_t)MD*DM);
   short* dbhi = allocS((size_t)MD*DM);  short* dblo = allocS((size_t)MD*DM);
   short* dahi = allocS((size_t)MD*DM);  short* dalo = allocS((size_t)MD*DM);
   short* dmhi = allocS((size_t)MD*DFFN);short* dmlo = allocS((size_t)MD*DFFN);
   float* opart= alloc((size_t)BB*NH*CSPLIT*NSTEP*DKH);
   float* mlp  = alloc((size_t)BB*NH*CSPLIT*2*NSTEP);
+  unsigned* barp = (unsigned*)alloc(4);
 
   const size_t MM = (size_t)DM*DM;
   short* dwq = (short*)t0;
@@ -711,6 +771,7 @@
   cvt(x,    xshi, xslo, (size_t)BT*64);
   cvt(in_W, iwhi, iwlo, (size_t)DM*64);
   zero_kernel<<<(MD*DM+255)/256, 256, 0, stream>>>(tok, MD*DM);
+  zero_u32<<<1, 64, 0, stream>>>(barp);
 
   gemm_split<0,0><<<dim3(BT/128, DM/128), 256, 0, stream>>>(
       xshi, xslo, iwhi, iwlo, in_b, h, (short*)nullptr, (short*)nullptr, BT, DM, 64);
@@ -760,51 +821,11 @@
   cvt(ffd_W1, fw1h, fw1l, (size_t)DFFN*DM);
   cvt(ffd_W2, fw2h, fw2l, (size_t)DM*DFFN);
 
-  #define GD(MRv, grid, ...) do { switch(MRv){ \
-    case 1: gemm_dec<1><<<grid,256,0,stream>>>(__VA_ARGS__); break; \
-    case 2: gemm_dec<2><<<grid,256,0,stream>>>(__VA_ARGS__); break; \
-    case 3: gemm_dec<3><<<grid,256,0,stream>>>(__VA_ARGS__); break; \
-    case 4: gemm_dec<4><<<grid,256,0,stream>>>(__VA_ARGS__); break; \
-    case 5: gemm_dec<5><<<grid,256,0,stream>>>(__VA_ARGS__); break; \
-    default: gemm_dec<6><<<grid,256,0,stream>>>(__VA_ARGS__); break; } } while(0)
-
-  for (int s=0; s<NSTEP; ++s) {
-    const int n = s+1;
-    const int rows = 4*n;
-    const int Mt = (rows + 15) & ~15;
-    const int MR = Mt >> 4;
-    dec_prep_split<<<rows,256,0,stream>>>(dbhi, dblo, tok);
-    for (int l=0; l<NL; ++l) {
-      const size_t bo_ = (size_t)l*DM;
-      short* qh = dwq + (size_t)l*2*MM; short* ql = qh + MM;
-      short* kh = dwk + (size_t)l*2*MM; short* kl = kh + MM;
-      short* vh = dwv + (size_t)l*2*MM; short* vl = vh + MM;
-      short* oh = dwo + (size_t)l*2*MM; short* ol = oh + MM;
-      GD(MR, dim3(8,8,3), dbhi,dblo, qh,ql, kh,kl, vh,vl, part, DM, DM, 8);
-      reduce_dec<0,0><<<dim3(Mt*4,3),256,0,stream>>>(part, dec_bq+bo_, dec_bk+bo_, dec_bv+bo_,
-          dq, dk, dv_, (short*)nullptr, (short*)nullptr, DM, 8);
-      attn_dec_selfp<<<BB*NH,256,0,stream>>>(dq, dk, dv_, dahi, dalo, n);
-      GD(MR, dim3(8,8,1), dahi,dalo, oh,ol, oh,ol, oh,ol, part, DM, DM, 8);
-      reduce_dec<0,1><<<dim3(Mt*4,1),256,0,stream>>>(part, dec_bo+bo_, dec_bo+bo_, dec_bo+bo_,
-          (float*)nullptr,(float*)nullptr,(float*)nullptr, dbhi, dblo, DM, 8);
-      GD(MR, dim3(8,8,1), dbhi,dblo, qh,ql, qh,ql, qh,ql, part, DM, DM, 8);
-      reduce_dec<0,0><<<dim3(Mt*4,1),256,0,stream>>>(part, dec_bq+bo_, dec_bq+bo_, dec_bq+bo_,
-          dq, dq, dq, (short*)nullptr, (short*)nullptr, DM, 8);
-      attn_cross_part<<<dim3(CSPLIT, BB*NH),256,0,stream>>>(dq, kcb+(size_t)l*BT*DM,
-          vcb+(size_t)l*BT*DM, opart, mlp, n);
-      attn_cross_comb<<<dim3(BB*NH, 6),256,0,stream>>>(opart, mlp, dahi, dalo, n);
-      GD(MR, dim3(8,8,1), dahi,dalo, oh,ol, oh,ol, oh,ol, part, DM, DM, 8);
-      reduce_dec<0,2><<<dim3(Mt*4,1),256,0,stream>>>(part, dec_bo+bo_, dec_bo+bo_, dec_bo+bo_,
-          dbuf, dbuf, dbuf, dbhi, dblo, DM, 8);
-      GD(MR, dim3(32,8,1), dbhi,dblo, fw1h,fw1l, fw1h,fw1l, fw1h,fw1l, part, DFFN, DM, 8);
-      reduce_dec<1,1><<<dim3(Mt*16,1),256,0,stream>>>(part, ffd_b1, ffd_b1, ffd_b1,
-          (float*)nullptr,(float*)nullptr,(float*)nullptr, dmhi, dmlo, DFFN, 8);
-      GD(MR, dim3(8,16,1), dmhi,dmlo, fw2h,fw2l, fw2h,fw2l, fw2h,fw2l, part, DM, DFFN, 16);
-      reduce_dec<0,0><<<dim3(Mt*4,1),256,0,stream>>>(part, ffd_b2, ffd_b2, ffd_b2,
-          dffo, dffo, dffo, (short*)nullptr, (short*)nullptr, DM, 16);
-      ln_add_dec<<<rows,256,0,stream>>>(dbuf, dffo, nd_g, nd_b, dbuf, dbhi, dblo);
-    }
-    out_step<<<BB,256,0,stream>>>(dbuf, out_W, out_b, temb_W, temb_b, dout, tok, s);
-  }
-  #undef GD
-}
+  dec_persist<<<NB, 256, 0, stream>>>(
+      dwq, dwk, dwv, dwo, fw1h, fw1l, fw2h, fw2l,
+      dec_bq, dec_bk, dec_bv, dec_bo, ffd_b1, ffd_b2,
+      kcb, vcb, nd_g, nd_b, out_W, out_b, temb_W, temb_b,
+      dout, tok, dbuf, dq, dk, dv_,
+      dbhi, dblo, dahi, dalo, dmhi, dmlo,
+      part, opart, mlp, barp);
+}
```

Result: slower. 50.92 ms (+208.6%).
